# Kernel tuning notes

Measured on AMD Instinct MI355X. Metric: run time of the kernel, lower is better.

## Reference

```python
import jax, jax.numpy as jnp
import numpy as np

DATA_WIDTH = 8  # fixed-point data width; bitstream length L = 2**DATA_WIDTH


def gen_bitstream(x, rng, data_width):
    """Vectorized GenBitstreamGroup.

    For each element x: if x == 0 -> Zero flag set, all-zero bitstream.
    Otherwise normalize |x| into [0.5, 1) via leftShift (number of left
    shifts), then unary-encode the normalized value against the RNG
    sequence: bit_t = 1 iff rng[t] < floor(norm * L).
    Returns (bits [..., L], leftShift [...], zero [...]).
    """
    L = rng.shape[0]
    zero = (x == 0)
    ax = jnp.abs(x)
    safe = jnp.where(zero, jnp.float32(1.0), ax)
    # leftShift: smallest s >= 0 with |x| * 2**s in [0.5, 1)
    s = jnp.clip(jnp.floor(-jnp.log2(safe)), 0.0, jnp.float32(data_width))
    norm = ax * jnp.exp2(s)                       # normalized magnitude in [0.5, 1]
    thresh = jnp.floor(norm * L)                  # integer threshold in [0, L]
    bits = (rng.astype(jnp.float32)[None, None, :] < thresh[:, :, None]).astype(jnp.float32)
    bits = jnp.where(zero[:, :, None], jnp.float32(0.0), bits)
    return bits, s, zero


def setup_inputs() -> dict:
    key = jax.random.key(0)
    k1, k2 = jax.random.split(key)
    M, K, N = 256, 256, 256
    L = 2 ** DATA_WIDTH
    tensor_1 = jax.random.uniform(k1, (M, K), dtype=jnp.float32)
    tensor_2 = jax.random.uniform(k2, (K, N), dtype=jnp.float32)
    rngSeq = jnp.arange(L, dtype=jnp.int32)
    return {"tensor_1": tensor_1, "tensor_2": tensor_2, "rngSeq": rngSeq}


def reference(tensor_1, tensor_2, rngSeq):
    L = rngSeq.shape[0]
    ascending = jnp.arange(L, dtype=jnp.int32)  # module's ascendingSeq for tensor_2
    b1, s1, z1 = gen_bitstream(tensor_1, rngSeq, DATA_WIDTH)      # [M,K,L]
    b2, s2, z2 = gen_bitstream(tensor_2, ascending, DATA_WIDTH)   # [K,N,L]
    # BitstreamMUL: AND the two bitstreams, popcount, rescale by bitstream
    # length and undo the normalization left-shifts.
    count = jnp.einsum('mkl,knl->mnk', b1, b2)                    # [M,N,K] popcounts
    scale = jnp.exp2(-(s1[:, None, :] + s2.T[None, :, :])) / L    # [M,N,K]
    valid = ((~z1)[:, None, :] & (~z2).T[None, :, :]).astype(jnp.float32)
    sgn = jnp.sign(tensor_1)[:, None, :] * jnp.sign(tensor_2).T[None, :, :]
    sc = count * scale * valid * sgn                              # per-k SC products
    return sc.sum(axis=-1)                                        # [M,N] result
```

## Files before the change

kernel.cpp:

```cpp
#include <hip/hip_runtime.h>


constexpr int DIM = 256;

__device__ inline void pack2(float v, float& tf, float& af) {
    float ax = fabsf(v);
    int   E;
    float fm = frexpf(ax, &E);
    int s = (fm == 0.5f ? 1 : 0) - E;
    s = s < 0 ? 0 : (s > 8 ? 8 : s);
    tf = floorf(ldexpf(ax, s + 8));
    tf = fminf(tf, 256.0f);
    af = ldexpf(copysignf(1.0f, v), -s);
}

__global__ __launch_bounds__(1024) void scgemm_fused(
    const float* __restrict__ x1, const float* __restrict__ x2,
    float* __restrict__ out)
{
    __shared__ float sT[DIM];
    __shared__ float sF[DIM];
    __shared__ float part[16][DIM];

    const int tid = threadIdx.x;
    const int m   = blockIdx.x;

    if (tid < DIM) {
        float tf, af;
        pack2(x1[m * DIM + tid], tf, af);
        sT[tid] = tf;
        sF[tid] = af;
    }
    __syncthreads();

    const int n0 = (tid & 63) * 4;
    const int kc = tid >> 6;
    const float4* __restrict__ x2v = (const float4*)x2;

    float acc0 = 0.f, acc1 = 0.f, acc2 = 0.f, acc3 = 0.f;
    #pragma unroll 4
    for (int kk = 0; kk < 16; ++kk) {
        const int k = kc * 16 + kk;
        float4 v = x2v[(k * DIM + n0) >> 2];
        float t0, a0, t1, a1, t2, a2, t3, a3;
        pack2(v.x, t0, a0);
        pack2(v.y, t1, a1);
        pack2(v.z, t2, a2);
        pack2(v.w, t3, a3);
        const float T1 = sT[k];
        const float F1 = sF[k];
        acc0 = fmaf(fminf(T1, t0), F1 * a0, acc0);
        acc1 = fmaf(fminf(T1, t1), F1 * a1, acc1);
        acc2 = fmaf(fminf(T1, t2), F1 * a2, acc2);
        acc3 = fmaf(fminf(T1, t3), F1 * a3, acc3);
    }
    *(float4*)&part[kc][n0] = make_float4(acc0, acc1, acc2, acc3);
    __syncthreads();

    if (tid < DIM) {
        float r = 0.f;
        #pragma unroll
        for (int c = 0; c < 16; ++c) r += part[c][tid];
        out[m * DIM + tid] = r * (1.0f / 256.0f);
    }
}

extern "C" void kernel_launch(void* const* d_in, const int* in_sizes, int n_in,
                              void* d_out, int out_size, void* d_ws, size_t ws_size,
                              hipStream_t stream)
{
    const float* x1  = (const float*)d_in[0];
    const float* x2  = (const float*)d_in[1];
    float* out = (float*)d_out;

    hipLaunchKernelGGL(scgemm_fused, dim3(DIM), dim3(1024), 0, stream, x1, x2, out);
}
```

Baseline: 65.57 us.

## Tile output into 16x16 blocks with shared packed operands and shuffle reduction

Each block now computes a 16x16 output tile instead of a full row. It packs both operand tiles into padded shared memory once, so each element of the second matrix is packed once per block instead of once per output row. Each thread accumulates a 4x4 register tile across a strided slice of k, and the partial sums are reduced with wavefront xor-shuffles instead of a shared-memory pass. Blocks shrink to 256 threads, which lowers per-block parallelism and adds an all-k staging phase up front.

Result: faster. 62.34 us (-4.9%).

```diff
diff --git a/kernel.cpp b/kernel.cpp
--- a/kernel.cpp
+++ b/kernel.cpp
@@ -2,66 +2,98 @@
 
 
 constexpr int DIM = 256;
+constexpr int PAD = 257;
 
-__device__ inline void pack2(float v, float& tf, float& af) {
+__device__ inline float2 pack2(float v) {
     float ax = fabsf(v);
     int   E;
     float fm = frexpf(ax, &E);
     int s = (fm == 0.5f ? 1 : 0) - E;
     s = s < 0 ? 0 : (s > 8 ? 8 : s);
-    tf = floorf(ldexpf(ax, s + 8));
+    float tf = floorf(ldexpf(ax, s + 8));
     tf = fminf(tf, 256.0f);
-    af = ldexpf(copysignf(1.0f, v), -s);
+    float af = ldexpf(copysignf(1.0f, v), -s);
+    return make_float2(tf, af);
 }
 
-__global__ __launch_bounds__(1024) void scgemm_fused(
+__global__ __launch_bounds__(256, 1) void scgemm_fused(
     const float* __restrict__ x1, const float* __restrict__ x2,
     float* __restrict__ out)
 {
-    __shared__ float sT[DIM];
-    __shared__ float sF[DIM];
-    __shared__ float part[16][DIM];
+    __shared__ float2 sP1[16 * PAD];
+    __shared__ float2 sP2[16 * PAD];
 
-    const int tid = threadIdx.x;
-    const int m   = blockIdx.x;
+    const int t  = threadIdx.x;
+    const int m0 = (blockIdx.x >> 4) * 16;
+    const int n0 = (blockIdx.x & 15) * 16;
 
-    if (tid < DIM) {
-        float tf, af;
-        pack2(x1[m * DIM + tid], tf, af);
-        sT[tid] = tf;
-        sF[tid] = af;
+    {
+        const int r = t >> 4, seg = t & 15;
+        const float4* src = (const float4*)(x1 + (m0 + r) * DIM + seg * 16);
+        float v[16];
+        #pragma unroll
+        for (int u = 0; u < 4; ++u) {
+            float4 q = src[u];
+            v[4*u+0] = q.x; v[4*u+1] = q.y; v[4*u+2] = q.z; v[4*u+3] = q.w;
+        }
+        #pragma unroll
+        for (int j = 0; j < 16; ++j) {
+            int c = (j + seg) & 15;
+            sP1[r * PAD + seg * 16 + c] = pack2(v[c]);
+        }
+    }
+    {
+        const int q = t & 3;
+        #pragma unroll
+        for (int it = 0; it < 4; ++it) {
+            const int row = (t >> 2) + 64 * it;
+            float4 w4 = *(const float4*)(x2 + row * DIM + n0 + q * 4);
+            float vv[4] = {w4.x, w4.y, w4.z, w4.w};
+            #pragma unroll
+            for (int jj = 0; jj < 4; ++jj)
+                sP2[(q * 4 + jj) * PAD + row] = pack2(vv[jj]);
+        }
     }
     __syncthreads();
 
-    const int n0 = (tid & 63) * 4;
-    const int kc = tid >> 6;
-    const float4* __restrict__ x2v = (const float4*)x2;
+    const int w   = t >> 6;
+    const int l   = t & 63;
+    const int njg = l & 3;
+    const int ks  = l >> 2;
 
-    float acc0 = 0.f, acc1 = 0.f, acc2 = 0.f, acc3 = 0.f;
+    float acc[4][4] = {};
     #pragma unroll 4
-    for (int kk = 0; kk < 16; ++kk) {
-        const int k = kc * 16 + kk;
-        float4 v = x2v[(k * DIM + n0) >> 2];
-        float t0, a0, t1, a1, t2, a2, t3, a3;
-        pack2(v.x, t0, a0);
-        pack2(v.y, t1, a1);
-        pack2(v.z, t2, a2);
-        pack2(v.w, t3, a3);
-        const float T1 = sT[k];
-        const float F1 = sF[k];
-        acc0 = fmaf(fminf(T1, t0), F1 * a0, acc0);
-        acc1 = fmaf(fminf(T1, t1), F1 * a1, acc1);
-        acc2 = fmaf(fminf(T1, t2), F1 * a2, acc2);
-        acc3 = fmaf(fminf(T1, t3), F1 * a3, acc3);
+    for (int j = 0; j < 16; ++j) {
+        const int k = ks + 16 * j;
+        float2 p1[4], p2[4];
+        #pragma unroll
+        for (int i = 0; i < 4; ++i)  p1[i]  = sP1[(w * 4 + i) * PAD + k];
+        #pragma unroll
+        for (int jj = 0; jj < 4; ++jj) p2[jj] = sP2[(njg * 4 + jj) * PAD + k];
+        #pragma unroll
+        for (int i = 0; i < 4; ++i)
+            #pragma unroll
+            for (int jj = 0; jj < 4; ++jj)
+                acc[i][jj] = fmaf(fminf(p1[i].x, p2[jj].x),
+                                  p1[i].y * p2[jj].y, acc[i][jj]);
     }
-    *(float4*)&part[kc][n0] = make_float4(acc0, acc1, acc2, acc3);
-    __syncthreads();
 
-    if (tid < DIM) {
-        float r = 0.f;
+    #pragma unroll
+    for (int mask = 4; mask <= 32; mask <<= 1)
         #pragma unroll
-        for (int c = 0; c < 16; ++c) r += part[c][tid];
-        out[m * DIM + tid] = r * (1.0f / 256.0f);
+        for (int i = 0; i < 4; ++i)
+            #pragma unroll
+            for (int jj = 0; jj < 4; ++jj)
+                acc[i][jj] += __shfl_xor(acc[i][jj], mask, 64);
+
+    if (l < 4) {
+        #pragma unroll
+        for (int i = 0; i < 4; ++i) {
+            float4 o = make_float4(acc[i][0], acc[i][1], acc[i][2], acc[i][3]);
+            o.x *= (1.0f/256.0f); o.y *= (1.0f/256.0f);
+            o.z *= (1.0f/256.0f); o.w *= (1.0f/256.0f);
+            *(float4*)(out + (m0 + w * 4 + i) * DIM + n0 + l * 4) = o;
+        }
     }
 }
 
@@ -73,5 +105,5 @@
     const float* x2  = (const float*)d_in[1];
     float* out = (float*)d_out;
 
-    hipLaunchKernelGGL(scgemm_fused, dim3(DIM), dim3(1024), 0, stream, x1, x2, out);
+    hipLaunchKernelGGL(scgemm_fused, dim3(256), dim3(256), 0, stream, x1, x2, out);
 }
```
